# Kernel tuning notes

Measured on AMD Instinct MI355X. Metric: run time of the kernel, lower is better.

## Reference

```python
import jax, jax.numpy as jnp
import numpy as np

EPS = 1e-5
H, DH = 8, 8  # n_head, d_hidden


def setup_inputs() -> dict:
    key = jax.random.key(0)
    ks = jax.random.split(key, 6)
    B, N, L, D = 1, 512, 1024, 64
    s = 1.0 / np.sqrt(D)
    return {
        "msa": jax.random.normal(ks[0], (B, N, L, D), jnp.float32),
        "ln_w": jnp.ones((D,), jnp.float32),
        "ln_b": jnp.zeros((D,), jnp.float32),
        "Wq": jax.random.normal(ks[1], (D, H * DH), jnp.float32) * s,
        "Wk": jax.random.normal(ks[2], (D, DH), jnp.float32) * s,
        "Wv": jax.random.normal(ks[3], (D, DH), jnp.float32) * s,
        "Wg": jax.random.normal(ks[4], (D, H * DH), jnp.float32) * s,
        "bg": jnp.ones((H * DH,), jnp.float32),
        "Wout": jax.random.normal(ks[5], (D, D), jnp.float32) * s,
        "bout": jnp.zeros((D,), jnp.float32),
    }


def reference(msa, ln_w, ln_b, Wq, Wk, Wv, Wg, bg, Wout, bout):
    B, N, L, D = msa.shape
    # LayerNorm over d_msa
    mu = jnp.mean(msa, axis=-1, keepdims=True)
    var = jnp.mean(jnp.square(msa - mu), axis=-1, keepdims=True)
    x = (msa - mu) * jax.lax.rsqrt(var + EPS) * ln_w + ln_b

    # Global query: project, split heads, mean over the N (sequence) axis
    q = (x @ Wq).reshape(B, N, L, H, DH).mean(axis=1)  # (B, L, H, DH)
    k = x @ Wk  # (B, N, L, DH)
    v = x @ Wv  # (B, N, L, DH)
    gate = jax.nn.sigmoid(x @ Wg + bg)  # (B, N, L, H*DH)

    scale = 1.0 / np.sqrt(DH)
    # SDPA batched over (B, L): q_len = H, kv_len = N, head_dim = DH
    scores = jnp.einsum("blhd,bnld->blhn", q, k) * scale
    attn = jax.nn.softmax(scores, axis=-1)
    o = jnp.einsum("blhn,bnld->blhd", attn, v)  # (B, L, H, DH)
    o = o.reshape(B, 1, L, H * DH)  # broadcast over N via gate

    out = (gate * o) @ Wout + bout  # (B, N, L, D)
    return out
```

## Files before the change

kernel.cpp:

```cpp
#include <hip/hip_runtime.h>
#include <math.h>

#define DD 64
#define NN 512
#define LL 1024
#define EPSF 1e-5f
#define NCH 32

typedef short short8 __attribute__((ext_vector_type(8)));
typedef float f32x4 __attribute__((ext_vector_type(4)));

static __device__ __forceinline__ unsigned bf16_rne(float f) {
  unsigned u = __float_as_uint(f);
  return (u + 0x7FFFu + ((u >> 16) & 1u)) >> 16;
}
static __device__ __forceinline__ float bf16_hi_f(float f) {
  unsigned u = __float_as_uint(f);
  return __uint_as_float((u + 0x7FFFu + ((u >> 16) & 1u)) & 0xFFFF0000u);
}
static __device__ __forceinline__ unsigned cvt_pk_bf16(float a, float b) {
  unsigned r;
  asm("v_cvt_pk_bf16_f32 %0, %1, %2" : "=v"(r) : "v"(a), "v"(b));
  return r;
}

__global__ __launch_bounds__(256) void kW(const float* __restrict__ Wg,
                                          const float* __restrict__ Wout,
                                          unsigned* __restrict__ Bpk)
{
  const int idx = blockIdx.x * 256 + threadIdx.x;
  const int e2   = idx & 3;
  const int lane = (idx >> 2) & 63;
  const int ctkt = (idx >> 8) & 7;
  const int h    = (idx >> 11) & 1;
  const int mv   = (idx >> 12) & 1;
  const int col  = ((ctkt >> 1) << 4) | (lane & 15);
  const int k0   = ((ctkt & 1) << 5) + ((lane >> 4) << 3) + (e2 << 1);
  const float* W = mv ? Wout : Wg;
  const float w0 = W[k0 * DD + col];
  const float w1 = W[(k0 + 1) * DD + col];
  unsigned b0, b1;
  if (h == 0) { b0 = bf16_rne(w0); b1 = bf16_rne(w1); }
  else        { b0 = bf16_rne(w0 - bf16_hi_f(w0)); b1 = bf16_rne(w1 - bf16_hi_f(w1)); }
  Bpk[idx] = b0 | (b1 << 16);
}

__global__ __launch_bounds__(256, 4) void kA(
    const float* __restrict__ msa, const float* __restrict__ lnw, const float* __restrict__ lnb,
    const float* __restrict__ Wk, const float* __restrict__ Wv,
    float* __restrict__ kb, float* __restrict__ vb, float* __restrict__ xbarP,
    unsigned short* __restrict__ xnh)
{
  __shared__ float xc[4][16][68];
  const int t = threadIdx.x;
  const int lane = t & 63;
  const int w = t >> 6;
  const int l_loc = t & 15;
  const int n_loc = t >> 4;
  const int lt = blockIdx.x & 63;
  const int nc = blockIdx.x >> 6;
  const int l0 = lt * 16;
  const int n = nc * 16 + n_loc;
  const int l = l0 + l_loc;

  float X[DD];
  {
    const float4* rp = (const float4*)(msa + ((size_t)n * LL + l) * DD);
#pragma unroll
    for (int i = 0; i < 16; ++i) {
      const float4 f = rp[i];
      X[4*i+0] = f.x; X[4*i+1] = f.y; X[4*i+2] = f.z; X[4*i+3] = f.w;
    }
  }

  float s = 0.f, s2 = 0.f;
#pragma unroll
  for (int d = 0; d < DD; ++d) { s += X[d]; s2 = fmaf(X[d], X[d], s2); }
  const float mu = s * (1.f / DD);
  const float rs = rsqrtf(fmaf(-mu, mu, s2 * (1.f / DD)) + EPSF);

  float ka[8], va[8];
#pragma unroll
  for (int j = 0; j < 8; ++j) { ka[j] = 0.f; va[j] = 0.f; }
#pragma unroll
  for (int d = 0; d < DD; ++d) {
    const float xn = fmaf((X[d] - mu) * rs, lnw[d], lnb[d]);
    X[d] = xn;
#pragma unroll
    for (int j = 0; j < 8; ++j) {
      ka[j] = fmaf(xn, Wk[d * 8 + j], ka[j]);
      va[j] = fmaf(xn, Wv[d * 8 + j], va[j]);
    }
  }

  {
    float4* kp = (float4*)(kb + ((size_t)l * NN + n) * 8);
    float4* vp = (float4*)(vb + ((size_t)l * NN + n) * 8);
    kp[0] = make_float4(ka[0], ka[1], ka[2], ka[3]);
    kp[1] = make_float4(ka[4], ka[5], ka[6], ka[7]);
    vp[0] = make_float4(va[0], va[1], va[2], va[3]);
    vp[1] = make_float4(va[4], va[5], va[6], va[7]);
  }

  {
    uint4* xp = (uint4*)(xnh + ((size_t)n * LL + l) * DD);
#pragma unroll
    for (int i = 0; i < 8; ++i)
      xp[i] = make_uint4(cvt_pk_bf16(X[8*i+0], X[8*i+1]),
                         cvt_pk_bf16(X[8*i+2], X[8*i+3]),
                         cvt_pk_bf16(X[8*i+4], X[8*i+5]),
                         cvt_pk_bf16(X[8*i+6], X[8*i+7]));
  }

  {
    const bool hi1 = (lane & 16) != 0;
#pragma unroll
    for (int k = 0; k < 32; ++k) {
      const float keep = hi1 ? X[k + 32] : X[k];
      const float send = hi1 ? X[k] : X[k + 32];
      X[k] = keep + __shfl_xor(send, 16);
    }
    const bool hi2 = (lane & 32) != 0;
#pragma unroll
    for (int k = 0; k < 16; ++k) {
      const float keep = hi2 ? X[k + 16] : X[k];
      const float send = hi2 ? X[k] : X[k + 16];
      X[k] = keep + __shfl_xor(send, 32);
    }
  }
  const int d0 = ((lane >> 4) & 1) * 32 + (lane >> 5) * 16;
#pragma unroll
  for (int k = 0; k < 16; ++k) xc[w][l_loc][d0 + k] = X[k];
  __syncthreads();

#pragma unroll
  for (int j = 0; j < 4; ++j) {
    const int c = t * 4 + j;
    const int ll = c >> 6, d = c & 63;
    const float sv = xc[0][ll][d] + xc[1][ll][d] + xc[2][ll][d] + xc[3][ll][d];
    xbarP[((size_t)(l0 + ll) * NCH + nc) * DD + d] = sv;
  }
}

__global__ __launch_bounds__(512) void kB(
    const float* __restrict__ kb, const float* __restrict__ vb,
    const float* __restrict__ xbarP, const float* __restrict__ Wq,
    float* __restrict__ obT)
{
  __shared__ float xbL[DD];
  __shared__ float qs[DD];
  __shared__ float ks[NN * 9];
  __shared__ float vs[NN * 9];
  const int l = blockIdx.x;
  const int t = threadIdx.x;
  const int h = t >> 6;
  const int lane = t & 63;

  const float* kl = kb + (size_t)l * NN * 8;
  const float* vl = vb + (size_t)l * NN * 8;
#pragma unroll
  for (int i = 0; i < 8; ++i) {
    const int idx = i * 512 + t;
    const int n = idx >> 3, j = idx & 7;
    ks[n*9 + j] = kl[idx];
    vs[n*9 + j] = vl[idx];
  }
  if (t < DD) {
    float s = 0.f;
    for (int p = 0; p < NCH; ++p) s += xbarP[((size_t)l * NCH + p) * DD + t];
    xbL[t] = s * (1.f / NN);
  }
  __syncthreads();
  if (t < DD) {
    float acc = 0.f;
    for (int d = 0; d < DD; ++d) acc = fmaf(xbL[d], Wq[d*DD + t], acc);
    qs[t] = acc * 0.35355339059327373f;
  }
  __syncthreads();

  float sc[8];
  float m = -1e30f;
#pragma unroll
  for (int i = 0; i < 8; ++i) {
    const int n = i * 64 + lane;
    float s = 0.f;
#pragma unroll
    for (int d = 0; d < 8; ++d) s = fmaf(qs[h*8 + d], ks[n*9 + d], s);
    sc[i] = s;
    m = fmaxf(m, s);
  }
#pragma unroll
  for (int off = 32; off; off >>= 1) m = fmaxf(m, __shfl_xor(m, off));
  float ssum = 0.f;
#pragma unroll
  for (int i = 0; i < 8; ++i) { sc[i] = __expf(sc[i] - m); ssum += sc[i]; }
#pragma unroll
  for (int off = 32; off; off >>= 1) ssum += __shfl_xor(ssum, off);
  const float inv = 1.f / ssum;

  float oacc[8];
#pragma unroll
  for (int d = 0; d < 8; ++d) oacc[d] = 0.f;
#pragma unroll
  for (int i = 0; i < 8; ++i) {
    const int n = i * 64 + lane;
#pragma unroll
    for (int d = 0; d < 8; ++d) oacc[d] = fmaf(sc[i], vs[n*9 + d], oacc[d]);
  }
#pragma unroll
  for (int d = 0; d < 8; ++d) {
#pragma unroll
    for (int off = 32; off; off >>= 1) oacc[d] += __shfl_xor(oacc[d], off);
  }
  if (lane == 0) {
#pragma unroll
    for (int d = 0; d < 8; ++d)
      obT[(size_t)(h * 8 + d) * LL + l] = oacc[d] * inv;
  }
}

__global__ __launch_bounds__(256, 4) void kC(
    const unsigned short* __restrict__ xnh, const unsigned* __restrict__ Bpk,
    const float* __restrict__ bg, const float* __restrict__ obT,
    const float* __restrict__ bout, float* __restrict__ out)
{
  __shared__ unsigned short TH[128 * 72];
  __shared__ unsigned short TL[128 * 72];
  const int t = threadIdx.x;
  const int lane = t & 63;
  const int w = t >> 6;
  const int rbase = 32 * w;
  const size_t R0 = (size_t)blockIdx.x * 128;

  const short8* Bp = (const short8*)Bpk;

  f32x4 acc[2][4];
#pragma unroll
  for (int rt = 0; rt < 2; ++rt)
#pragma unroll
    for (int ct = 0; ct < 4; ++ct) acc[rt][ct] = f32x4{0.f, 0.f, 0.f, 0.f};

  {
    short8 ah[2][2];
#pragma unroll
    for (int rt = 0; rt < 2; ++rt) {
      const size_t ar = R0 + rbase + rt * 16 + (lane & 15);
      const int kg = (lane >> 4) * 8;
      ah[rt][0] = *(const short8*)&xnh[ar * DD + kg];
      ah[rt][1] = *(const short8*)&xnh[ar * DD + 32 + kg];
    }
#pragma unroll
    for (int ct = 0; ct < 4; ++ct) {
      const short8 bh0 = Bp[(0 * 8 + ct * 2 + 0) * 64 + lane];
      const short8 bh1 = Bp[(0 * 8 + ct * 2 + 1) * 64 + lane];
      const short8 bl0 = Bp[(1 * 8 + ct * 2 + 0) * 64 + lane];
      const short8 bl1 = Bp[(1 * 8 + ct * 2 + 1) * 64 + lane];
#pragma unroll
      for (int rt = 0; rt < 2; ++rt) {
        f32x4 c = acc[rt][ct];
        c = __builtin_amdgcn_mfma_f32_16x16x32_bf16(ah[rt][0], bh0, c, 0, 0, 0);
        c = __builtin_amdgcn_mfma_f32_16x16x32_bf16(ah[rt][1], bh1, c, 0, 0, 0);
        c = __builtin_amdgcn_mfma_f32_16x16x32_bf16(ah[rt][0], bl0, c, 0, 0, 0);
        c = __builtin_amdgcn_mfma_f32_16x16x32_bf16(ah[rt][1], bl1, c, 0, 0, 0);
        acc[rt][ct] = c;
      }
    }
  }

#pragma unroll
  for (int rt = 0; rt < 2; ++rt) {
    const int rl0 = rbase + rt * 16 + ((lane >> 4) << 2);
    const int li0 = (int)((R0 + rl0) & (LL - 1));
#pragma unroll
    for (int ct = 0; ct < 4; ++ct) {
      const int col = ct * 16 + (lane & 15);
      const float4 ov = *(const float4*)&obT[(size_t)col * LL + li0];
      const float bgc = bg[col];
      const float p0 = acc[rt][ct][0] + bgc;
      const float p1 = acc[rt][ct][1] + bgc;
      const float p2 = acc[rt][ct][2] + bgc;
      const float p3 = acc[rt][ct][3] + bgc;
      const float tv0 = ov.x / (1.f + __expf(-p0));
      const float tv1 = ov.y / (1.f + __expf(-p1));
      const float tv2 = ov.z / (1.f + __expf(-p2));
      const float tv3 = ov.w / (1.f + __expf(-p3));
      const unsigned ph01 = cvt_pk_bf16(tv0, tv1);
      const unsigned ph23 = cvt_pk_bf16(tv2, tv3);
      const float h0 = __uint_as_float(ph01 << 16);
      const float h1 = __uint_as_float(ph01 & 0xFFFF0000u);
      const float h2 = __uint_as_float(ph23 << 16);
      const float h3 = __uint_as_float(ph23 & 0xFFFF0000u);
      const unsigned pl01 = cvt_pk_bf16(tv0 - h0, tv1 - h1);
      const unsigned pl23 = cvt_pk_bf16(tv2 - h2, tv3 - h3);
      TH[(rl0 + 0) * 72 + col] = (unsigned short)ph01;
      TH[(rl0 + 1) * 72 + col] = (unsigned short)(ph01 >> 16);
      TH[(rl0 + 2) * 72 + col] = (unsigned short)ph23;
      TH[(rl0 + 3) * 72 + col] = (unsigned short)(ph23 >> 16);
      TL[(rl0 + 0) * 72 + col] = (unsigned short)pl01;
      TL[(rl0 + 1) * 72 + col] = (unsigned short)(pl01 >> 16);
      TL[(rl0 + 2) * 72 + col] = (unsigned short)pl23;
      TL[(rl0 + 3) * 72 + col] = (unsigned short)(pl23 >> 16);
    }
  }

#pragma unroll
  for (int rt = 0; rt < 2; ++rt)
#pragma unroll
    for (int ct = 0; ct < 4; ++ct) {
      const float bo = bout[ct * 16 + (lane & 15)];
      acc[rt][ct] = f32x4{bo, bo, bo, bo};
    }
  {
    short8 ah[2][2], al[2][2];
#pragma unroll
    for (int rt = 0; rt < 2; ++rt) {
      const int ar = rbase + rt * 16 + (lane & 15);
      const int kg = (lane >> 4) * 8;
      ah[rt][0] = *(const short8*)&TH[ar * 72 + kg];
      ah[rt][1] = *(const short8*)&TH[ar * 72 + 32 + kg];
      al[rt][0] = *(const short8*)&TL[ar * 72 + kg];
      al[rt][1] = *(const short8*)&TL[ar * 72 + 32 + kg];
    }
#pragma unroll
    for (int ct = 0; ct < 4; ++ct) {
      const short8 bh0 = Bp[(2 * 8 + ct * 2 + 0) * 64 + lane];
      const short8 bh1 = Bp[(2 * 8 + ct * 2 + 1) * 64 + lane];
      const short8 bl0 = Bp[(3 * 8 + ct * 2 + 0) * 64 + lane];
      const short8 bl1 = Bp[(3 * 8 + ct * 2 + 1) * 64 + lane];
#pragma unroll
      for (int rt = 0; rt < 2; ++rt) {
        f32x4 c = acc[rt][ct];
        c = __builtin_amdgcn_mfma_f32_16x16x32_bf16(ah[rt][0], bh0, c, 0, 0, 0);
        c = __builtin_amdgcn_mfma_f32_16x16x32_bf16(ah[rt][1], bh1, c, 0, 0, 0);
        c = __builtin_amdgcn_mfma_f32_16x16x32_bf16(ah[rt][0], bl0, c, 0, 0, 0);
        c = __builtin_amdgcn_mfma_f32_16x16x32_bf16(ah[rt][1], bl1, c, 0, 0, 0);
        c = __builtin_amdgcn_mfma_f32_16x16x32_bf16(al[rt][0], bh0, c, 0, 0, 0);
        c = __builtin_amdgcn_mfma_f32_16x16x32_bf16(al[rt][1], bh1, c, 0, 0, 0);
        acc[rt][ct] = c;
      }
    }
  }

#pragma unroll
  for (int rt = 0; rt < 2; ++rt) {
#pragma unroll
    for (int j = 0; j < 4; ++j) {
      const size_t rg = R0 + rbase + rt * 16 + ((lane >> 4) << 2) + j;
#pragma unroll
      for (int ct = 0; ct < 4; ++ct)
        out[rg * DD + ct * 16 + (lane & 15)] = acc[rt][ct][j];
    }
  }
}

extern "C" void kernel_launch(void* const* d_in, const int* in_sizes, int n_in,
                              void* d_out, int out_size, void* d_ws, size_t ws_size,
                              hipStream_t stream)
{
  const float* msa  = (const float*)d_in[0];
  const float* lnw  = (const float*)d_in[1];
  const float* lnb  = (const float*)d_in[2];
  const float* Wq   = (const float*)d_in[3];
  const float* Wk   = (const float*)d_in[4];
  const float* Wv   = (const float*)d_in[5];
  const float* Wg   = (const float*)d_in[6];
  const float* bg   = (const float*)d_in[7];
  const float* Wout = (const float*)d_in[8];
  const float* bout = (const float*)d_in[9];
  float* out = (float*)d_out;

  float* kb    = (float*)d_ws;
  float* vb    = kb + (size_t)LL * NN * 8;
  float* xbarP = vb + (size_t)LL * NN * 8;
  float* obT   = xbarP + (size_t)LL * NCH * DD;
  unsigned* Bpk = (unsigned*)(obT + (size_t)DD * LL);
  unsigned short* xnh = (unsigned short*)(Bpk + 8192);

  kW<<<32, 256, 0, stream>>>(Wg, Wout, Bpk);
  kA<<<64 * NCH, 256, 0, stream>>>(msa, lnw, lnb, Wk, Wv, kb, vb, xbarP, xnh);
  kB<<<LL, 512, 0, stream>>>(kb, vb, xbarP, Wq, obT);
  kC<<<(NN * LL) / 128, 256, 0, stream>>>(xnh, Bpk, bg, obT, bout, out);
}
```

Before: 137.1 us.

## Store normalized MSA in d-group-major bf16 layout and use software bf16 rounding

The normalized bf16 activations are now written in a layout where each 8-element d-group is contiguous across l (index (n*8+g)*LL+l). Consecutive lanes then write and read adjacent 16-byte chunks in both the producer and the MFMA consumer, which should coalesce global stores and loads better. The inline-asm packed bf16 conversion is replaced by a software round-to-nearest-even helper, and the LayerNorm affine step is folded into one fma with precomputed scale and offset. The software rounding costs extra integer ALU work per element compared with the hardware pack instruction.

Result: faster. 128.4 us (-6.4%).

```diff
diff --git a/kernel.cpp b/kernel.cpp
--- a/kernel.cpp
+++ b/kernel.cpp
@@ -17,11 +17,6 @@
 static __device__ __forceinline__ float bf16_hi_f(float f) {
   unsigned u = __float_as_uint(f);
   return __uint_as_float((u + 0x7FFFu + ((u >> 16) & 1u)) & 0xFFFF0000u);
-}
-static __device__ __forceinline__ unsigned cvt_pk_bf16(float a, float b) {
-  unsigned r;
-  asm("v_cvt_pk_bf16_f32 %0, %1, %2" : "=v"(r) : "v"(a), "v"(b));
-  return r;
 }
 
 __global__ __launch_bounds__(256) void kW(const float* __restrict__ Wg,
@@ -78,19 +73,32 @@
   for (int d = 0; d < DD; ++d) { s += X[d]; s2 = fmaf(X[d], X[d], s2); }
   const float mu = s * (1.f / DD);
   const float rs = rsqrtf(fmaf(-mu, mu, s2 * (1.f / DD)) + EPSF);
+  const float aa = rs, bb = -mu * rs;
 
   float ka[8], va[8];
 #pragma unroll
   for (int j = 0; j < 8; ++j) { ka[j] = 0.f; va[j] = 0.f; }
-#pragma unroll
-  for (int d = 0; d < DD; ++d) {
-    const float xn = fmaf((X[d] - mu) * rs, lnw[d], lnb[d]);
-    X[d] = xn;
-#pragma unroll
-    for (int j = 0; j < 8; ++j) {
-      ka[j] = fmaf(xn, Wk[d * 8 + j], ka[j]);
-      va[j] = fmaf(xn, Wv[d * 8 + j], va[j]);
-    }
+
+  uint4* xg = (uint4*)xnh;
+#pragma unroll
+  for (int g = 0; g < 8; ++g) {
+#pragma unroll
+    for (int e = 0; e < 8; ++e) {
+      const int d = 8 * g + e;
+      const float xn = fmaf(fmaf(X[d], aa, bb), lnw[d], lnb[d]);
+      X[d] = xn;
+#pragma unroll
+      for (int j = 0; j < 8; ++j) {
+        ka[j] = fmaf(xn, Wk[d * 8 + j], ka[j]);
+        va[j] = fmaf(xn, Wv[d * 8 + j], va[j]);
+      }
+    }
+    uint4 q;
+    q.x = bf16_rne(X[8*g+0]) | (bf16_rne(X[8*g+1]) << 16);
+    q.y = bf16_rne(X[8*g+2]) | (bf16_rne(X[8*g+3]) << 16);
+    q.z = bf16_rne(X[8*g+4]) | (bf16_rne(X[8*g+5]) << 16);
+    q.w = bf16_rne(X[8*g+6]) | (bf16_rne(X[8*g+7]) << 16);
+    xg[(size_t)(n * 8 + g) * LL + l] = q;
   }
 
   {
@@ -103,16 +111,6 @@
   }
 
   {
-    uint4* xp = (uint4*)(xnh + ((size_t)n * LL + l) * DD);
-#pragma unroll
-    for (int i = 0; i < 8; ++i)
-      xp[i] = make_uint4(cvt_pk_bf16(X[8*i+0], X[8*i+1]),
-                         cvt_pk_bf16(X[8*i+2], X[8*i+3]),
-                         cvt_pk_bf16(X[8*i+4], X[8*i+5]),
-                         cvt_pk_bf16(X[8*i+6], X[8*i+7]));
-  }
-
-  {
     const bool hi1 = (lane & 16) != 0;
 #pragma unroll
     for (int k = 0; k < 32; ++k) {
@@ -128,9 +126,9 @@
       X[k] = keep + __shfl_xor(send, 32);
     }
   }
-  const int d0 = ((lane >> 4) & 1) * 32 + (lane >> 5) * 16;
-#pragma unroll
-  for (int k = 0; k < 16; ++k) xc[w][l_loc][d0 + k] = X[k];
+  const int d0i = ((lane >> 4) & 1) * 32 + (lane >> 5) * 16;
+#pragma unroll
+  for (int k = 0; k < 16; ++k) xc[w][l_loc][d0i + k] = X[k];
   __syncthreads();
 
 #pragma unroll
@@ -231,8 +229,11 @@
   const int w = t >> 6;
   const int rbase = 32 * w;
   const size_t R0 = (size_t)blockIdx.x * 128;
+  const int nblk = (int)(R0 >> 10);
+  const int lbase = (int)(R0 & (LL - 1));
 
   const short8* Bp = (const short8*)Bpk;
+  const short8* Xp = (const short8*)xnh;
 
   f32x4 acc[2][4];
 #pragma unroll
@@ -244,10 +245,10 @@
     short8 ah[2][2];
 #pragma unroll
     for (int rt = 0; rt < 2; ++rt) {
-      const size_t ar = R0 + rbase + rt * 16 + (lane & 15);
-      const int kg = (lane >> 4) * 8;
-      ah[rt][0] = *(const short8*)&xnh[ar * DD + kg];
-      ah[rt][1] = *(const short8*)&xnh[ar * DD + 32 + kg];
+      const int ar_l = lbase + rbase + rt * 16 + (lane & 15);
+      const int g = lane >> 4;
+      ah[rt][0] = Xp[(size_t)(nblk * 8 + g) * LL + ar_l];
+      ah[rt][1] = Xp[(size_t)(nblk * 8 + 4 + g) * LL + ar_l];
     }
 #pragma unroll
     for (int ct = 0; ct < 4; ++ct) {
@@ -276,30 +277,17 @@
       const int col = ct * 16 + (lane & 15);
       const float4 ov = *(const float4*)&obT[(size_t)col * LL + li0];
       const float bgc = bg[col];
-      const float p0 = acc[rt][ct][0] + bgc;
-      const float p1 = acc[rt][ct][1] + bgc;
-      const float p2 = acc[rt][ct][2] + bgc;
-      const float p3 = acc[rt][ct][3] + bgc;
-      const float tv0 = ov.x / (1.f + __expf(-p0));
-      const float tv1 = ov.y / (1.f + __expf(-p1));
-      const float tv2 = ov.z / (1.f + __expf(-p2));
-      const float tv3 = ov.w / (1.f + __expf(-p3));
-      const unsigned ph01 = cvt_pk_bf16(tv0, tv1);
-      const unsigned ph23 = cvt_pk_bf16(tv2, tv3);
-      const float h0 = __uint_as_float(ph01 << 16);
-      const float h1 = __uint_as_float(ph01 & 0xFFFF0000u);
-      const float h2 = __uint_as_float(ph23 << 16);
-      const float h3 = __uint_as_float(ph23 & 0xFFFF0000u);
-      const unsigned pl01 = cvt_pk_bf16(tv0 - h0, tv1 - h1);
-      const unsigned pl23 = cvt_pk_bf16(tv2 - h2, tv3 - h3);
-      TH[(rl0 + 0) * 72 + col] = (unsigned short)ph01;
-      TH[(rl0 + 1) * 72 + col] = (unsigned short)(ph01 >> 16);
-      TH[(rl0 + 2) * 72 + col] = (unsigned short)ph23;
-      TH[(rl0 + 3) * 72 + col] = (unsigned short)(ph23 >> 16);
-      TL[(rl0 + 0) * 72 + col] = (unsigned short)pl01;
-      TL[(rl0 + 1) * 72 + col] = (unsigned short)(pl01 >> 16);
-      TL[(rl0 + 2) * 72 + col] = (unsigned short)pl23;
-      TL[(rl0 + 3) * 72 + col] = (unsigned short)(pl23 >> 16);
+#define SIG_STORE(j, ocomp)                                             \
+      {                                                                 \
+        const float pre = acc[rt][ct][j] + bgc;                         \
+        const float tv = (ocomp) / (1.f + __expf(-pre));                \
+        const unsigned hb = bf16_rne(tv);                               \
+        TH[(rl0 + (j)) * 72 + col] = (unsigned short)hb;                \
+        const float rvl = tv - __uint_as_float(hb << 16);               \
+        TL[(rl0 + (j)) * 72 + col] = (unsigned short)bf16_rne(rvl);     \
+      }
+      SIG_STORE(0, ov.x) SIG_STORE(1, ov.y) SIG_STORE(2, ov.z) SIG_STORE(3, ov.w)
+#undef SIG_STORE
     }
   }
 
```
